# Kernel tuning notes

Measured on AMD Instinct MI355X. Metric: run time of the kernel, lower is better.

Reference implementation:

```python
import jax, jax.numpy as jnp
import numpy as np

TH = 1.0            # q_threshold for all IF neurons
POS_MAX = 7.0       # level//2 - 1, level=16, sym=True
NEG_MIN = -8.0      # -(level//2)
PREFIRE = 0.2       # attn_softmax_IF.prefire
S_QUANT = 7.0       # spiking_softmax scale = level//2 - 1
NUM_HEADS = 8


def if_step(x, vmem0, acc0, th=TH, pos_max=POS_MAX, neg_min=NEG_MIN):
    """One timestep of a symmetric ST-BIF neuron with straight-through surrogate.
    Forward: spike in {-1,0,+1}*th gated by membrane and accumulator saturation.
    Backward: identity (STE), accumulator is a constant."""
    acc0f = acc0.astype(x.dtype)
    v = vmem0 + x
    pos = jnp.logical_and(v >= th, acc0f < pos_max)
    neg = jnp.logical_and(v < 0.0, acc0f > neg_min)
    spike = pos.astype(x.dtype) - neg.astype(x.dtype)
    out_hard = spike * th
    out = x + jax.lax.stop_gradient(out_hard - x)  # STE: fwd=spike*th, bwd=identity
    acc = jax.lax.stop_gradient(acc0f + spike)     # running spike count (constant wrt grads)
    return out, acc


def setup_inputs() -> dict:
    key = jax.random.key(0)
    ks = jax.random.split(key, 16)
    B, N, C, H = 4, 1024, 512, NUM_HEADS
    D = C // H
    f32 = jnp.float32
    inp = {
        "x": jax.random.normal(ks[0], (B, N, C), dtype=f32),
        "w_qkv": jax.random.normal(ks[1], (3 * C, C), dtype=f32) * 0.02,
        "b_qkv": jnp.zeros((3 * C,), dtype=f32),
        "w_proj": jax.random.normal(ks[2], (C, C), dtype=f32) * 0.02,
        "b_proj": jnp.zeros((C,), dtype=f32),
        "q_vmem": jax.random.uniform(ks[3], (B, H, N, D), dtype=f32),
        "k_vmem": jax.random.uniform(ks[4], (B, H, N, D), dtype=f32),
        "v_vmem": jax.random.uniform(ks[5], (B, H, N, D), dtype=f32),
        "attn_vmem": jax.random.uniform(ks[6], (B, H, N, N), dtype=f32),
        "q_acc0": jax.random.randint(ks[7], (B, H, N, D), 0, 8).astype(jnp.int32),
        "k_acc0": jax.random.randint(ks[8], (B, H, N, D), 0, 8).astype(jnp.int32),
        "v_acc0": jax.random.randint(ks[9], (B, H, N, D), 0, 8).astype(jnp.int32),
        "attn_acc0": jax.random.randint(ks[10], (B, H, N, N), 0, 8).astype(jnp.int32),
    }
    return inp


def reference(x, w_qkv, b_qkv, w_proj, b_proj,
              q_vmem, k_vmem, v_vmem, attn_vmem,
              q_acc0, k_acc0, v_acc0, attn_acc0):
    B, N, C = x.shape
    H = NUM_HEADS
    D = C // H
    scale = D ** -0.5
    sg = jax.lax.stop_gradient

    # qkv projection -> [3, B, H, N, D]
    qkv = (x @ w_qkv.T + b_qkv).reshape(B, N, 3, H, D).transpose(2, 0, 3, 1, 4)
    q_in, k_in, v_in = qkv[0], qkv[1], qkv[2]

    # ST-BIF IF neurons (one timestep, carried state)
    q_s, q_acc = if_step(q_in, q_vmem, q_acc0)
    k_s, k_acc = if_step(k_in, k_vmem, k_acc0)
    v_s, v_acc = if_step(v_in, v_vmem, v_acc0)

    q = q_s * scale
    # accumulator corrections: acc_q * q_threshold (*scale for q) minus detached spike output
    q_corr = sg(q_acc * TH * scale - q)
    k_corr = sg(k_acc * TH - k_s)
    v_corr = sg(v_acc * TH - v_s)

    # multi: (q + q_corr) @ k^T + q @ k_corr^T   -> [B, H, N, N]
    attn = (jnp.einsum('bhnd,bhmd->bhnm', q + q_corr, k_s)
            + jnp.einsum('bhnd,bhmd->bhnm', q, k_corr))

    # spiking softmax substitute: softmax of the (accumulated) scores, scaled to quant range
    attn = jax.nn.softmax(attn, axis=-1) * S_QUANT

    # attn_softmax_IF with prefire bias on the membrane
    attn_s, attn_acc = if_step(attn, attn_vmem + PREFIRE * TH, attn_acc0)
    attn_corr = sg(attn_acc * TH - attn_s)

    # multi1: (attn + attn_corr) @ v + attn @ v_corr  -> [B, H, N, D]
    out = (jnp.einsum('bhnm,bhmd->bhnd', attn_s + attn_corr, v_s)
           + jnp.einsum('bhnm,bhmd->bhnd', attn_s, v_corr))

    # after_attn_IF: fresh state (rounding init 0.5*th, zero accumulator)
    out, _ = if_step(out, jnp.asarray(0.5 * TH, out.dtype), jnp.zeros_like(out))

    out = out.transpose(0, 2, 1, 3).reshape(B, N, C)
    return out @ w_proj.T + b_proj
```

## Files before the change

### kernel.cpp

```cpp
#include <hip/hip_runtime.h>
#include <hip/hip_bf16.h>
#include <cstdint>

typedef short short8 __attribute__((ext_vector_type(8)));
typedef float f32x4 __attribute__((ext_vector_type(4)));
typedef int   int4v __attribute__((ext_vector_type(4)));

using bf16 = __hip_bfloat16;

#define MFMA16(a, b, c) __builtin_amdgcn_mfma_f32_16x16x32_bf16((a), (b), (c), 0, 0, 0)
#define MFMAI8(a, b, c) __builtin_amdgcn_mfma_i32_16x16x64_i8((a), (b), (c), 0, 0, 0)

__device__ __forceinline__ short8 ldb8(const bf16* p) {
    return *reinterpret_cast<const short8*>(p);
}
__device__ __forceinline__ unsigned pk4(int a, int b, int c, int d) {
    return (a & 255) | ((b & 255) << 8) | ((c & 255) << 16) | ((d & 255) << 24);
}

__global__ __launch_bounds__(256) void k_cast(const float* __restrict__ src,
                                              bf16* __restrict__ dst, int n)
{
    for (int i = blockIdx.x * 256 + threadIdx.x; i < n; i += gridDim.x * 256)
        dst[i] = __float2bfloat16(src[i]);
}

__global__ __launch_bounds__(256, 3) void k_qkv_f32(
    const float* __restrict__ X, const float* __restrict__ W, const float* __restrict__ bq,
    const float* __restrict__ qvm, const float* __restrict__ kvm, const float* __restrict__ vvm,
    const int* __restrict__ qac, const int* __restrict__ kac, const int* __restrict__ vac,
    int8_t* __restrict__ Q2, int8_t* __restrict__ K2c, int8_t* __restrict__ VsT, int8_t* __restrict__ VaT)
{
    __shared__ float As[16][64];
    __shared__ float Bs[16][128];
    const int tid = threadIdx.x;
    const int r0 = blockIdx.y * 64;
    const int c0 = blockIdx.x * 128;
    const int tm = (tid & 15) * 4;
    const int tn = (tid >> 4) * 8;
    const int arow = tid >> 2, ak = (tid & 3) * 4;
    const int brow = tid >> 1, bk = (tid & 1) * 8;

    float acc[4][8] = {};
    for (int kk = 0; kk < 512; kk += 16) {
        const float4 a4 = *reinterpret_cast<const float4*>(X + (size_t)(r0 + arow) * 512 + kk + ak);
        const float4 w0 = *reinterpret_cast<const float4*>(W + (size_t)(c0 + brow) * 512 + kk + bk);
        const float4 w1 = *reinterpret_cast<const float4*>(W + (size_t)(c0 + brow) * 512 + kk + bk + 4);
        __syncthreads();
        As[ak + 0][arow] = a4.x; As[ak + 1][arow] = a4.y; As[ak + 2][arow] = a4.z; As[ak + 3][arow] = a4.w;
        Bs[bk + 0][brow] = w0.x; Bs[bk + 1][brow] = w0.y; Bs[bk + 2][brow] = w0.z; Bs[bk + 3][brow] = w0.w;
        Bs[bk + 4][brow] = w1.x; Bs[bk + 5][brow] = w1.y; Bs[bk + 6][brow] = w1.z; Bs[bk + 7][brow] = w1.w;
        __syncthreads();
        #pragma unroll
        for (int k = 0; k < 16; ++k) {
            const float4 av = *reinterpret_cast<const float4*>(&As[k][tm]);
            const float4 bv0 = *reinterpret_cast<const float4*>(&Bs[k][tn]);
            const float4 bv1 = *reinterpret_cast<const float4*>(&Bs[k][tn + 4]);
            const float ar[4] = {av.x, av.y, av.z, av.w};
            const float br[8] = {bv0.x, bv0.y, bv0.z, bv0.w, bv1.x, bv1.y, bv1.z, bv1.w};
            #pragma unroll
            for (int i = 0; i < 4; ++i)
                #pragma unroll
                for (int j = 0; j < 8; ++j)
                    acc[i][j] += ar[i] * br[j];
        }
    }

    const int sel = c0 >> 9;
    const int h   = ((c0 + tn) & 511) >> 6;
    const int d0  = (c0 + tn) & 63;
    const float4 bb0 = *reinterpret_cast<const float4*>(bq + c0 + tn);
    const float4 bb1 = *reinterpret_cast<const float4*>(bq + c0 + tn + 4);
    const float bcol[8] = {bb0.x, bb0.y, bb0.z, bb0.w, bb1.x, bb1.y, bb1.z, bb1.w};

    const float* VM = (sel == 0) ? qvm : (sel == 1) ? kvm : vvm;
    const int*   AC = (sel == 0) ? qac : (sel == 1) ? kac : vac;
    float vmv[4][8]; int acv[4][8]; int bhn[4];
    #pragma unroll
    for (int i = 0; i < 4; ++i) {
        const int r = r0 + tm + i;
        const int b = r >> 10, n = r & 1023;
        const int bh = b * 8 + h;
        bhn[i] = bh * 1024 + n;
        const size_t i4 = (size_t)bhn[i] * 64 + d0;
        const float4 v0 = *reinterpret_cast<const float4*>(VM + i4);
        const float4 v1 = *reinterpret_cast<const float4*>(VM + i4 + 4);
        const int4  c0i = *reinterpret_cast<const int4*>(AC + i4);
        const int4  c1i = *reinterpret_cast<const int4*>(AC + i4 + 4);
        vmv[i][0]=v0.x; vmv[i][1]=v0.y; vmv[i][2]=v0.z; vmv[i][3]=v0.w;
        vmv[i][4]=v1.x; vmv[i][5]=v1.y; vmv[i][6]=v1.z; vmv[i][7]=v1.w;
        acv[i][0]=c0i.x; acv[i][1]=c0i.y; acv[i][2]=c0i.z; acv[i][3]=c0i.w;
        acv[i][4]=c1i.x; acv[i][5]=c1i.y; acv[i][6]=c1i.z; acv[i][7]=c1i.w;
    }

    int spm[4][8];
    #pragma unroll
    for (int i = 0; i < 4; ++i)
        #pragma unroll
        for (int j = 0; j < 8; ++j) {
            const float v_ = vmv[i][j] + (acc[i][j] + bcol[j]);
            int sp = ((v_ >= 1.0f) && (acv[i][j] < 7)) ? 1 : 0;
            if (v_ < 0.0f) sp -= 1;
            spm[i][j] = sp;
        }

    if (sel == 2) {
        #pragma unroll
        for (int j = 0; j < 8; ++j) {
            const int nb = (r0 & 1023) + tm;
            const unsigned us = pk4(spm[0][j], spm[1][j], spm[2][j], spm[3][j]);
            const unsigned ua = pk4(acv[0][j], acv[1][j], acv[2][j], acv[3][j]);
            const size_t vi = ((size_t)((bhn[0] >> 10) * 64 + d0 + j)) * 1024 + nb;
            *reinterpret_cast<unsigned*>(VsT + vi) = us;
            *reinterpret_cast<unsigned*>(VaT + vi) = ua;
        }
    } else {
        #pragma unroll
        for (int i = 0; i < 4; ++i) {
            int v0[8], v1[8];
            #pragma unroll
            for (int j = 0; j < 8; ++j) {
                if (sel == 0) { v0[j] = acv[i][j] + spm[i][j]; v1[j] = spm[i][j]; }
                else          { v0[j] = spm[i][j];             v1[j] = acv[i][j]; }
            }
            uint2 a, b;
            a.x = pk4(v0[0], v0[1], v0[2], v0[3]); a.y = pk4(v0[4], v0[5], v0[6], v0[7]);
            b.x = pk4(v1[0], v1[1], v1[2], v1[3]); b.y = pk4(v1[4], v1[5], v1[6], v1[7]);
            int8_t* base = ((sel == 0) ? Q2 : K2c) + (size_t)bhn[i] * 128 + d0;
            *reinterpret_cast<uint2*>(base)      = a;
            *reinterpret_cast<uint2*>(base + 64) = b;
        }
    }
}

__global__ __launch_bounds__(256, 4) void k_attn(
    const int8_t* __restrict__ Q2, const int8_t* __restrict__ K2c,
    const float* __restrict__ avm, const int* __restrict__ aac,
    const int8_t* __restrict__ VsT, const int8_t* __restrict__ VaT,
    bf16* __restrict__ O2)
{
    __shared__ alignas(16) char Sc[32768];
    short* const Ss = (short*)Sc;
    const int w = threadIdx.x >> 6, lane = threadIdx.x & 63;
    const int lo = lane & 15, hi = lane >> 4;
    const int h = blockIdx.y, bb = blockIdx.z;
    const int bh = bb * 8 + h;
    const int n0 = blockIdx.x * 16;

    {
        const int8_t* qb = Q2 + ((size_t)(bh * 1024 + n0 + lo)) * 128 + hi * 16;
        const int4v a0 = *reinterpret_cast<const int4v*>(qb);
        const int4v a1 = *reinterpret_cast<const int4v*>(qb + 64);
        const int8_t* kbp = K2c + ((size_t)(bh * 1024 + w * 256 + lo)) * 128 + hi * 16;
        int4v b0 = *reinterpret_cast<const int4v*>(kbp);
        int4v b1 = *reinterpret_cast<const int4v*>(kbp + 64);
        for (int t = 0; t < 16; ++t) {
            const int4v c0f = b0, c1f = b1;
            if (t < 15) {
                kbp += 16 * 128;
                b0 = *reinterpret_cast<const int4v*>(kbp);
                b1 = *reinterpret_cast<const int4v*>(kbp + 64);
            }
            int4v acc = {0, 0, 0, 0};
            acc = MFMAI8(a0, c0f, acc);
            acc = MFMAI8(a1, c1f, acc);
            const int cc = w * 256 + t * 16 + lo;
            short* sb = Ss + ((cc >> 9) << 13) + (cc & 511);
            #pragma unroll
            for (int r = 0; r < 4; ++r)
                sb[(hi * 4 + r) << 9] = (short)acc[r];
        }
    }

    const int row = threadIdx.x >> 4, q = threadIdx.x & 15;
    const size_t gRow = ((size_t)bh * 1024 + (n0 + row)) * 1024;

#define LOADJ(j, VM0, VM1, AC0, AC1) {                                          \
        const int cb_ = (q + 16 * (j)) * 8;                                     \
        VM0 = *reinterpret_cast<const float4*>(avm + gRow + cb_);               \
        VM1 = *reinterpret_cast<const float4*>(avm + gRow + cb_ + 4);           \
        AC0 = *reinterpret_cast<const int4*>(aac + gRow + cb_);                 \
        AC1 = *reinterpret_cast<const int4*>(aac + gRow + cb_ + 4); }

    float4 vmA0, vmA1, vmB0, vmB1, vmC0, vmC1;
    int4   acA0, acA1, acB0, acB1, acC0, acC1;
    LOADJ(0, vmA0, vmA1, acA0, acA1);
    LOADJ(1, vmB0, vmB1, acB0, acB1);

    __syncthreads();

    short8 sc[8];
    #pragma unroll
    for (int j = 0; j < 8; ++j) {
        const int kb = q + 16 * j;
        sc[j] = *reinterpret_cast<const short8*>(Sc + ((kb >> 6) << 14) + (row << 10) + ((kb & 63) << 4));
    }
    __syncthreads();

    LOADJ(2, vmC0, vmC1, acC0, acC1);

    int mxi = sc[0][0];
    #pragma unroll
    for (int j = 0; j < 8; ++j)
        #pragma unroll
        for (int i = 0; i < 8; ++i)
            mxi = max(mxi, (int)sc[j][i]);
    float mx = 0.125f * (float)mxi;
    mx = fmaxf(mx, __shfl_xor(mx, 1));
    mx = fmaxf(mx, __shfl_xor(mx, 2));
    mx = fmaxf(mx, __shfl_xor(mx, 4));
    mx = fmaxf(mx, __shfl_xor(mx, 8));

    float sum = 0.f;
    #pragma unroll
    for (int j = 0; j < 8; ++j)
        #pragma unroll
        for (int i = 0; i < 8; ++i)
            sum += expf(0.125f * (float)sc[j][i] - mx);
    sum += __shfl_xor(sum, 1);
    sum += __shfl_xor(sum, 2);
    sum += __shfl_xor(sum, 4);
    sum += __shfl_xor(sum, 8);

#define PSTEP(j, VM0, VM1, AC0, AC1) {                                          \
        const float vmr_[8] = {VM0.x, VM0.y, VM0.z, VM0.w,                      \
                               VM1.x, VM1.y, VM1.z, VM1.w};                     \
        const int aar_[8] = {AC0.x, AC0.y, AC0.z, AC0.w,                        \
                             AC1.x, AC1.y, AC1.z, AC1.w};                       \
        unsigned p1u[8], p2u[8];                                                \
        _Pragma("unroll")                                                       \
        for (int i = 0; i < 8; ++i) {                                           \
            const float e_ = expf(0.125f * (float)sc[j][i] - mx);               \
            const float p7 = (e_ / sum) * 7.0f;                                 \
            const float v_ = (vmr_[i] + 0.2f) + p7;          \
            const int a0i = aar_[i];                              \
            const int sp = ((v_ >= 1.0f) && (a0i < 7)) ? 1 : 0;                 \
            p1u[i] = (unsigned)(a0i + sp);                                      \
            p2u[i] = (unsigned)sp;                                              \
        }                                                                       \
        uint2 w1, w2;                                                           \
        w1.x = p1u[0] | (p1u[1] << 8) | (p1u[2] << 16) | (p1u[3] << 24);        \
        w1.y = p1u[4] | (p1u[5] << 8) | (p1u[6] << 16) | (p1u[7] << 24);        \
        w2.x = p2u[0] | (p2u[1] << 8) | (p2u[2] << 16) | (p2u[3] << 24);        \
        w2.y = p2u[4] | (p2u[5] << 8) | (p2u[6] << 16) | (p2u[7] << 24);        \
        const int kb = q + 16 * (j);                                            \
        char* pb = Sc + (row << 10) + (((kb << 3) ^ ((row & 7) << 4)));         \
        *reinterpret_cast<uint2*>(pb)         = w1;                             \
        *reinterpret_cast<uint2*>(pb + 16384) = w2; }

    PSTEP(0, vmA0, vmA1, acA0, acA1);
    LOADJ(3, vmA0, vmA1, acA0, acA1);
    PSTEP(1, vmB0, vmB1, acB0, acB1);
    LOADJ(4, vmB0, vmB1, acB0, acB1);
    PSTEP(2, vmC0, vmC1, acC0, acC1);
    LOADJ(5, vmC0, vmC1, acC0, acC1);
    PSTEP(3, vmA0, vmA1, acA0, acA1);
    LOADJ(6, vmA0, vmA1, acA0, acA1);
    PSTEP(4, vmB0, vmB1, acB0, acB1);
    LOADJ(7, vmB0, vmB1, acB0, acB1);
    PSTEP(5, vmC0, vmC1, acC0, acC1);
    PSTEP(6, vmA0, vmA1, acA0, acA1);
    PSTEP(7, vmB0, vmB1, acB0, acB1);

    __syncthreads();

    {
        const int d0 = w * 16;
        const int8_t* vs = VsT + ((size_t)(bh * 64 + d0 + lo)) * 1024 + hi * 16;
        const int8_t* va = VaT + ((size_t)(bh * 64 + d0 + lo)) * 1024 + hi * 16;
        int4v nvs = *reinterpret_cast<const int4v*>(vs);
        int4v nva = *reinterpret_cast<const int4v*>(va);
        int4v acc = {0, 0, 0, 0};
        for (int tt = 0; tt < 16; ++tt) {
            const int4v cvs = nvs, cva = nva;
            if (tt < 15) {
                nvs = *reinterpret_cast<const int4v*>(vs + (tt + 1) * 64);
                nva = *reinterpret_cast<const int4v*>(va + (tt + 1) * 64);
            }
            const int off = (tt * 64 + hi * 16) ^ ((lo & 7) << 4);
            const char* pb = Sc + (lo << 10) + off;
            const int4v a1 = *reinterpret_cast<const int4v*>(pb);
            const int4v a2 = *reinterpret_cast<const int4v*>(pb + 16384);
            acc = MFMAI8(a1, cvs, acc);
            acc = MFMAI8(a2, cva, acc);
        }
        #pragma unroll
        for (int r = 0; r < 4; ++r) {
            const int n = n0 + hi * 4 + r;
            const float o = (float)acc[r];
            const float o2 = (o >= 0.5f ? 1.f : 0.f) - (o < -0.5f ? 1.f : 0.f);
            O2[((size_t)(bb * 1024 + n)) * 512 + h * 64 + d0 + lo] = __float2bfloat16(o2);
        }
    }
#undef LOADJ
#undef PSTEP
}

__global__ __launch_bounds__(256) void k_proj(
    const bf16* __restrict__ O2, const bf16* __restrict__ W, const float* __restrict__ bias,
    float* __restrict__ Y)
{
    const int w = threadIdx.x >> 6, lane = threadIdx.x & 63;
    const int lo = lane & 15, hi = lane >> 4;
    const int r0 = blockIdx.y * 16;
    const int c0 = blockIdx.x * 256 + w * 64;

    f32x4 acc[4] = {{0.f,0.f,0.f,0.f},{0.f,0.f,0.f,0.f},{0.f,0.f,0.f,0.f},{0.f,0.f,0.f,0.f}};
    const bf16* op = O2 + (size_t)(r0 + lo) * 512 + hi * 8;
    #pragma unroll 4
    for (int kb = 0; kb < 16; ++kb) {
        short8 a = ldb8(op + kb * 32);
        #pragma unroll
        for (int t = 0; t < 4; ++t) {
            short8 b = ldb8(W + (size_t)(c0 + t * 16 + lo) * 512 + kb * 32 + hi * 8);
            acc[t] = MFMA16(a, b, acc[t]);
        }
    }
    #pragma unroll
    for (int t = 0; t < 4; ++t) {
        const int col = c0 + t * 16 + lo;
        const float bcol = bias[col];
        #pragma unroll
        for (int r = 0; r < 4; ++r) {
            const int rr = r0 + hi * 4 + r;
            Y[(size_t)rr * 512 + col] = acc[t][r] + bcol;
        }
    }
}

extern "C" void kernel_launch(void* const* d_in, const int* in_sizes, int n_in,
                              void* d_out, int out_size, void* d_ws, size_t ws_size,
                              hipStream_t stream)
{
    const float* x     = (const float*)d_in[0];
    const float* wqkv  = (const float*)d_in[1];
    const float* bqkv  = (const float*)d_in[2];
    const float* wproj = (const float*)d_in[3];
    const float* bproj = (const float*)d_in[4];
    const float* qvm   = (const float*)d_in[5];
    const float* kvm   = (const float*)d_in[6];
    const float* vvm   = (const float*)d_in[7];
    const float* avm   = (const float*)d_in[8];
    const int*   qac   = (const int*)d_in[9];
    const int*   kac   = (const int*)d_in[10];
    const int*   vac   = (const int*)d_in[11];
    const int*   aac   = (const int*)d_in[12];

    char* p = (char*)d_ws;
    int8_t* Q2  = (int8_t*)p; p += (size_t)32 * 1024 * 128;
    int8_t* K2c = (int8_t*)p; p += (size_t)32 * 1024 * 128;
    int8_t* VsT = (int8_t*)p; p += (size_t)32 * 64 * 1024;
    int8_t* VaT = (int8_t*)p; p += (size_t)32 * 64 * 1024;
    bf16*   O2  = (bf16*)p;   p += (size_t)4096 * 512 * 2;
    bf16*   Wp  = (bf16*)p;   p += (size_t)512 * 512 * 2;

    k_cast<<<dim3(256), 256, 0, stream>>>(wproj, Wp, 512 * 512);
    k_qkv_f32<<<dim3(12, 64), 256, 0, stream>>>(x, wqkv, bqkv, qvm, kvm, vvm,
                                                qac, kac, vac, Q2, K2c, VsT, VaT);
    k_attn<<<dim3(64, 8, 4), 256, 0, stream>>>(Q2, K2c, avm, aac, VsT, VaT, O2);
    k_proj<<<dim3(2, 256), 256, 0, stream>>>(O2, Wp, bproj, (float*)d_out);
}
```

Measured before the change: 511.6 us.

## Replace FP32 SIMT QKV GEMM with split-FP16 MFMA emulation

The QKV projection moves from a scalar FP32 shared-memory GEMM to FP16 MFMA instructions. Inputs and weights are split into scaled high and low FP16 parts, so that three MFMA products approximate FP32 accuracy. A new prep kernel does the splitting and also folds in the bf16 cast of the projection weight. This removes a compute-bound FP32 FMA loop, but adds an extra pass that writes the split copies. The epilogue now uses scattered per-element loads and stores, and precision could differ slightly near spike thresholds.

```diff
diff --git a/kernel.cpp b/kernel.cpp
--- a/kernel.cpp
+++ b/kernel.cpp
@@ -5,130 +5,133 @@
 typedef short short8 __attribute__((ext_vector_type(8)));
 typedef float f32x4 __attribute__((ext_vector_type(4)));
 typedef int   int4v __attribute__((ext_vector_type(4)));
+typedef _Float16 fp16x8 __attribute__((ext_vector_type(8)));
 
 using bf16 = __hip_bfloat16;
 
 #define MFMA16(a, b, c) __builtin_amdgcn_mfma_f32_16x16x32_bf16((a), (b), (c), 0, 0, 0)
 #define MFMAI8(a, b, c) __builtin_amdgcn_mfma_i32_16x16x64_i8((a), (b), (c), 0, 0, 0)
+#define MFMAF16(a, b, c) __builtin_amdgcn_mfma_f32_16x16x32_f16((a), (b), (c), 0, 0, 0)
 
 __device__ __forceinline__ short8 ldb8(const bf16* p) {
     return *reinterpret_cast<const short8*>(p);
 }
-__device__ __forceinline__ unsigned pk4(int a, int b, int c, int d) {
-    return (a & 255) | ((b & 255) << 8) | ((c & 255) << 16) | ((d & 255) << 24);
-}
-
-__global__ __launch_bounds__(256) void k_cast(const float* __restrict__ src,
-                                              bf16* __restrict__ dst, int n)
-{
-    for (int i = blockIdx.x * 256 + threadIdx.x; i < n; i += gridDim.x * 256)
-        dst[i] = __float2bfloat16(src[i]);
-}
-
-__global__ __launch_bounds__(256, 3) void k_qkv_f32(
-    const float* __restrict__ X, const float* __restrict__ W, const float* __restrict__ bq,
+
+__global__ __launch_bounds__(256) void k_prep(
+    const float* __restrict__ X, const float* __restrict__ W, const float* __restrict__ Wp,
+    _Float16* __restrict__ Xh, _Float16* __restrict__ Xl,
+    _Float16* __restrict__ Wh, _Float16* __restrict__ Wl, bf16* __restrict__ Wpb)
+{
+    const int NX = 4096 * 512, NW = 1536 * 512, NP = 512 * 512;
+    for (int i = blockIdx.x * 256 + threadIdx.x; i < NX + NW + NP; i += gridDim.x * 256) {
+        if (i < NX) {
+            const float v = X[i] * 512.0f;
+            const _Float16 h = (_Float16)v;
+            Xh[i] = h;
+            Xl[i] = (_Float16)((v - (float)h) * 2048.0f);
+        } else if (i < NX + NW) {
+            const int j = i - NX;
+            const float v = W[j] * 512.0f;
+            const _Float16 h = (_Float16)v;
+            Wh[j] = h;
+            Wl[j] = (_Float16)((v - (float)h) * 2048.0f);
+        } else {
+            const int j = i - NX - NW;
+            Wpb[j] = __float2bfloat16(Wp[j]);
+        }
+    }
+}
+
+__global__ __launch_bounds__(256, 3) void k_qkv_f16(
+    const _Float16* __restrict__ Xh, const _Float16* __restrict__ Xl,
+    const _Float16* __restrict__ Wh, const _Float16* __restrict__ Wl,
+    const float* __restrict__ bq,
     const float* __restrict__ qvm, const float* __restrict__ kvm, const float* __restrict__ vvm,
     const int* __restrict__ qac, const int* __restrict__ kac, const int* __restrict__ vac,
-    int8_t* __restrict__ Q2, int8_t* __restrict__ K2c, int8_t* __restrict__ VsT, int8_t* __restrict__ VaT)
-{
-    __shared__ float As[16][64];
-    __shared__ float Bs[16][128];
+    int8_t* __restrict__ Q2, int8_t* __restrict__ K2c,
+    int8_t* __restrict__ VsT, int8_t* __restrict__ VaT)
+{
     const int tid = threadIdx.x;
-    const int r0 = blockIdx.y * 64;
-    const int c0 = blockIdx.x * 128;
-    const int tm = (tid & 15) * 4;
-    const int tn = (tid >> 4) * 8;
-    const int arow = tid >> 2, ak = (tid & 3) * 4;
-    const int brow = tid >> 1, bk = (tid & 1) * 8;
-
-    float acc[4][8] = {};
-    for (int kk = 0; kk < 512; kk += 16) {
-        const float4 a4 = *reinterpret_cast<const float4*>(X + (size_t)(r0 + arow) * 512 + kk + ak);
-        const float4 w0 = *reinterpret_cast<const float4*>(W + (size_t)(c0 + brow) * 512 + kk + bk);
-        const float4 w1 = *reinterpret_cast<const float4*>(W + (size_t)(c0 + brow) * 512 + kk + bk + 4);
-        __syncthreads();
-        As[ak + 0][arow] = a4.x; As[ak + 1][arow] = a4.y; As[ak + 2][arow] = a4.z; As[ak + 3][arow] = a4.w;
-        Bs[bk + 0][brow] = w0.x; Bs[bk + 1][brow] = w0.y; Bs[bk + 2][brow] = w0.z; Bs[bk + 3][brow] = w0.w;
-        Bs[bk + 4][brow] = w1.x; Bs[bk + 5][brow] = w1.y; Bs[bk + 6][brow] = w1.z; Bs[bk + 7][brow] = w1.w;
-        __syncthreads();
-        #pragma unroll
-        for (int k = 0; k < 16; ++k) {
-            const float4 av = *reinterpret_cast<const float4*>(&As[k][tm]);
-            const float4 bv0 = *reinterpret_cast<const float4*>(&Bs[k][tn]);
-            const float4 bv1 = *reinterpret_cast<const float4*>(&Bs[k][tn + 4]);
-            const float ar[4] = {av.x, av.y, av.z, av.w};
-            const float br[8] = {bv0.x, bv0.y, bv0.z, bv0.w, bv1.x, bv1.y, bv1.z, bv1.w};
-            #pragma unroll
-            for (int i = 0; i < 4; ++i)
-                #pragma unroll
-                for (int j = 0; j < 8; ++j)
-                    acc[i][j] += ar[i] * br[j];
-        }
-    }
-
-    const int sel = c0 >> 9;
-    const int h   = ((c0 + tn) & 511) >> 6;
-    const int d0  = (c0 + tn) & 63;
-    const float4 bb0 = *reinterpret_cast<const float4*>(bq + c0 + tn);
-    const float4 bb1 = *reinterpret_cast<const float4*>(bq + c0 + tn + 4);
-    const float bcol[8] = {bb0.x, bb0.y, bb0.z, bb0.w, bb1.x, bb1.y, bb1.z, bb1.w};
-
+    const int w = tid >> 6, lane = tid & 63, lo = lane & 15, hi = lane >> 4;
+    const int wr = w >> 1, wc = w & 1;
+    const int r0 = blockIdx.y * 64 + wr * 32;
+    const int c0 = blockIdx.x * 128 + wc * 64;
+
+    f32x4 hh[2][4] = {};
+    f32x4 md[2][4] = {};
+
+    const _Float16* xhp = Xh + (size_t)(r0 + lo) * 512 + hi * 8;
+    const _Float16* xlp = Xl + (size_t)(r0 + lo) * 512 + hi * 8;
+    const _Float16* whp = Wh + (size_t)(c0 + lo) * 512 + hi * 8;
+    const _Float16* wlp = Wl + (size_t)(c0 + lo) * 512 + hi * 8;
+
+    for (int kc = 0; kc < 16; ++kc) {
+        const int ko = kc * 32;
+        const fp16x8 Ah0 = *reinterpret_cast<const fp16x8*>(xhp + ko);
+        const fp16x8 Ah1 = *reinterpret_cast<const fp16x8*>(xhp + ko + 16 * 512);
+        const fp16x8 Al0 = *reinterpret_cast<const fp16x8*>(xlp + ko);
+        const fp16x8 Al1 = *reinterpret_cast<const fp16x8*>(xlp + ko + 16 * 512);
+        fp16x8 Bh[4], Bl[4];
+        #pragma unroll
+        for (int j = 0; j < 4; ++j) {
+            Bh[j] = *reinterpret_cast<const fp16x8*>(whp + ko + j * 16 * 512);
+            Bl[j] = *reinterpret_cast<const fp16x8*>(wlp + ko + j * 16 * 512);
+        }
+        #pragma unroll
+        for (int j = 0; j < 4; ++j) {
+            hh[0][j] = MFMAF16(Ah0, Bh[j], hh[0][j]);
+            hh[1][j] = MFMAF16(Ah1, Bh[j], hh[1][j]);
+            md[0][j] = MFMAF16(Ah0, Bl[j], md[0][j]);
+            md[0][j] = MFMAF16(Al0, Bh[j], md[0][j]);
+            md[1][j] = MFMAF16(Ah1, Bl[j], md[1][j]);
+            md[1][j] = MFMAF16(Al1, Bh[j], md[1][j]);
+        }
+    }
+
+    const int sel = (unsigned)c0 >> 9;
     const float* VM = (sel == 0) ? qvm : (sel == 1) ? kvm : vvm;
     const int*   AC = (sel == 0) ? qac : (sel == 1) ? kac : vac;
-    float vmv[4][8]; int acv[4][8]; int bhn[4];
-    #pragma unroll
-    for (int i = 0; i < 4; ++i) {
-        const int r = r0 + tm + i;
-        const int b = r >> 10, n = r & 1023;
-        const int bh = b * 8 + h;
-        bhn[i] = bh * 1024 + n;
-        const size_t i4 = (size_t)bhn[i] * 64 + d0;
-        const float4 v0 = *reinterpret_cast<const float4*>(VM + i4);
-        const float4 v1 = *reinterpret_cast<const float4*>(VM + i4 + 4);
-        const int4  c0i = *reinterpret_cast<const int4*>(AC + i4);
-        const int4  c1i = *reinterpret_cast<const int4*>(AC + i4 + 4);
-        vmv[i][0]=v0.x; vmv[i][1]=v0.y; vmv[i][2]=v0.z; vmv[i][3]=v0.w;
-        vmv[i][4]=v1.x; vmv[i][5]=v1.y; vmv[i][6]=v1.z; vmv[i][7]=v1.w;
-        acv[i][0]=c0i.x; acv[i][1]=c0i.y; acv[i][2]=c0i.z; acv[i][3]=c0i.w;
-        acv[i][4]=c1i.x; acv[i][5]=c1i.y; acv[i][6]=c1i.z; acv[i][7]=c1i.w;
-    }
-
-    int spm[4][8];
-    #pragma unroll
-    for (int i = 0; i < 4; ++i)
-        #pragma unroll
-        for (int j = 0; j < 8; ++j) {
-            const float v_ = vmv[i][j] + (acc[i][j] + bcol[j]);
-            int sp = ((v_ >= 1.0f) && (acv[i][j] < 7)) ? 1 : 0;
-            if (v_ < 0.0f) sp -= 1;
-            spm[i][j] = sp;
-        }
-
-    if (sel == 2) {
-        #pragma unroll
-        for (int j = 0; j < 8; ++j) {
-            const int nb = (r0 & 1023) + tm;
-            const unsigned us = pk4(spm[0][j], spm[1][j], spm[2][j], spm[3][j]);
-            const unsigned ua = pk4(acv[0][j], acv[1][j], acv[2][j], acv[3][j]);
-            const size_t vi = ((size_t)((bhn[0] >> 10) * 64 + d0 + j)) * 1024 + nb;
-            *reinterpret_cast<unsigned*>(VsT + vi) = us;
-            *reinterpret_cast<unsigned*>(VaT + vi) = ua;
-        }
-    } else {
-        #pragma unroll
-        for (int i = 0; i < 4; ++i) {
-            int v0[8], v1[8];
+
+    #pragma unroll
+    for (int i = 0; i < 2; ++i) {
+        const int rowb = r0 + i * 16 + hi * 4;
+        const int b = rowb >> 10, nb = rowb & 1023;
+        #pragma unroll
+        for (int j = 0; j < 4; ++j) {
+            const int c = c0 + j * 16 + lo;
+            const int ch = c & 511;
+            const int hh_ = ch >> 6, d = ch & 63;
+            const int bh = b * 8 + hh_;
+            const float bcol = bq[c];
+            int sp[4], a4[4];
             #pragma unroll
-            for (int j = 0; j < 8; ++j) {
-                if (sel == 0) { v0[j] = acv[i][j] + spm[i][j]; v1[j] = spm[i][j]; }
-                else          { v0[j] = spm[i][j];             v1[j] = acv[i][j]; }
+            for (int r = 0; r < 4; ++r) {
+                const size_t gi = (size_t)(bh * 1024 + nb + r) * 64 + d;
+                const float vm = VM[gi];
+                const int a0 = AC[gi];
+                const float val = fmaf(md[i][j][r], 0x1p-11f, hh[i][j][r]) * 0x1p-18f;
+                const float v_ = vm + (val + bcol);
+                int s = ((v_ >= 1.0f) && (a0 < 7)) ? 1 : 0;
+                if (v_ < 0.0f) s -= 1;
+                sp[r] = s; a4[r] = a0;
             }
-            uint2 a, b;
-            a.x = pk4(v0[0], v0[1], v0[2], v0[3]); a.y = pk4(v0[4], v0[5], v0[6], v0[7]);
-            b.x = pk4(v1[0], v1[1], v1[2], v1[3]); b.y = pk4(v1[4], v1[5], v1[6], v1[7]);
-            int8_t* base = ((sel == 0) ? Q2 : K2c) + (size_t)bhn[i] * 128 + d0;
-            *reinterpret_cast<uint2*>(base)      = a;
-            *reinterpret_cast<uint2*>(base + 64) = b;
+            if (sel == 2) {
+                uchar4 us, ua;
+                us.x = (uint8_t)sp[0]; us.y = (uint8_t)sp[1]; us.z = (uint8_t)sp[2]; us.w = (uint8_t)sp[3];
+                ua.x = (uint8_t)a4[0]; ua.y = (uint8_t)a4[1]; ua.z = (uint8_t)a4[2]; ua.w = (uint8_t)a4[3];
+                const size_t vi = (size_t)(bh * 64 + d) * 1024 + nb;
+                *reinterpret_cast<uchar4*>(VsT + vi) = us;
+                *reinterpret_cast<uchar4*>(VaT + vi) = ua;
+            } else {
+                int8_t* base = ((sel == 0) ? Q2 : K2c) + (size_t)(bh * 1024 + nb) * 128 + d;
+                #pragma unroll
+                for (int r = 0; r < 4; ++r) {
+                    const int v0 = (sel == 0) ? a4[r] + sp[r] : sp[r];
+                    const int v1 = (sel == 0) ? sp[r]         : a4[r];
+                    base[r * 128]      = (int8_t)v0;
+                    base[r * 128 + 64] = (int8_t)v1;
+                }
+            }
         }
     }
 }
@@ -347,16 +350,20 @@
     const int*   aac   = (const int*)d_in[12];
 
     char* p = (char*)d_ws;
-    int8_t* Q2  = (int8_t*)p; p += (size_t)32 * 1024 * 128;
-    int8_t* K2c = (int8_t*)p; p += (size_t)32 * 1024 * 128;
-    int8_t* VsT = (int8_t*)p; p += (size_t)32 * 64 * 1024;
-    int8_t* VaT = (int8_t*)p; p += (size_t)32 * 64 * 1024;
-    bf16*   O2  = (bf16*)p;   p += (size_t)4096 * 512 * 2;
-    bf16*   Wp  = (bf16*)p;   p += (size_t)512 * 512 * 2;
-
-    k_cast<<<dim3(256), 256, 0, stream>>>(wproj, Wp, 512 * 512);
-    k_qkv_f32<<<dim3(12, 64), 256, 0, stream>>>(x, wqkv, bqkv, qvm, kvm, vvm,
+    int8_t*   Q2  = (int8_t*)p;   p += (size_t)32 * 1024 * 128;
+    int8_t*   K2c = (int8_t*)p;   p += (size_t)32 * 1024 * 128;
+    int8_t*   VsT = (int8_t*)p;   p += (size_t)32 * 64 * 1024;
+    int8_t*   VaT = (int8_t*)p;   p += (size_t)32 * 64 * 1024;
+    bf16*     O2  = (bf16*)p;     p += (size_t)4096 * 512 * 2;
+    bf16*     Wpb = (bf16*)p;     p += (size_t)512 * 512 * 2;
+    _Float16* Xh  = (_Float16*)p; p += (size_t)4096 * 512 * 2;
+    _Float16* Xl  = (_Float16*)p; p += (size_t)4096 * 512 * 2;
+    _Float16* Wh  = (_Float16*)p; p += (size_t)1536 * 512 * 2;
+    _Float16* Wl  = (_Float16*)p; p += (size_t)1536 * 512 * 2;
+
+    k_prep<<<dim3(2048), 256, 0, stream>>>(x, wqkv, wproj, Xh, Xl, Wh, Wl, Wpb);
+    k_qkv_f16<<<dim3(12, 64), 256, 0, stream>>>(Xh, Xl, Wh, Wl, bqkv, qvm, kvm, vvm,
                                                 qac, kac, vac, Q2, K2c, VsT, VaT);
     k_attn<<<dim3(64, 8, 4), 256, 0, stream>>>(Q2, K2c, avm, aac, VsT, VaT, O2);
-    k_proj<<<dim3(2, 256), 256, 0, stream>>>(O2, Wp, bproj, (float*)d_out);
-}
+    k_proj<<<dim3(2, 256), 256, 0, stream>>>(O2, Wpb, bproj, (float*)d_out);
+}
```

After: 459.7 us. 1.11x faster.
